# Performance work log

Hardware: AMD Instinct MI355X
Metric: run time of the kernel (lower is better)

Reference implementation:

```python
import jax, jax.numpy as jnp
import numpy as np

H = 16  # num_heads
EPS = 1e-6

def _sigma(t):
    # ELU(x)+1, the positive feature map used by Infini-attention linear memory
    return jax.nn.elu(t) + 1.0

def setup_inputs() -> dict:
    key = jax.random.key(0)
    ks = jax.random.split(key, 6)
    B, S, D = 1, 2048, 1024
    d = D // H
    std = 1.0 / np.sqrt(D)
    return {
        "x": jax.random.normal(ks[0], (B, S, D), dtype=jnp.float32),
        "M": jnp.zeros((H, d, d), dtype=jnp.float32),
        "z": jnp.zeros((H, d), dtype=jnp.float32),
        "Wq": jax.random.normal(ks[1], (D, D), dtype=jnp.float32) * std,
        "Wk": jax.random.normal(ks[2], (D, D), dtype=jnp.float32) * std,
        "Wv": jax.random.normal(ks[3], (D, D), dtype=jnp.float32) * std,
        "Wo": jax.random.normal(ks[4], (D, D), dtype=jnp.float32) * std,
        "beta": jnp.zeros((H,), dtype=jnp.float32),
    }

def reference(x, M, z, Wq, Wk, Wv, Wo, beta):
    B, S, D = x.shape
    d = D // H
    # projections -> [B, H, S, d]
    def proj(W):
        return (x @ W).reshape(B, S, H, d).transpose(0, 2, 1, 3)
    q, k, v = proj(Wq), proj(Wk), proj(Wv)

    # ---- local causal dot-product attention ----
    scale = 1.0 / jnp.sqrt(jnp.asarray(d, dtype=x.dtype))
    scores = jnp.einsum('bhqd,bhkd->bhqk', q, k) * scale  # [B,H,S,S]
    causal = jnp.tril(jnp.ones((S, S), dtype=bool))
    scores = jnp.where(causal, scores, jnp.asarray(-1e30, dtype=scores.dtype))
    A_dot = jnp.einsum('bhqk,bhkd->bhqd', jax.nn.softmax(scores, axis=-1), v)

    # ---- compressive memory retrieval (linear attention) ----
    sq = _sigma(q)                                       # [B,H,S,d]
    num = jnp.einsum('bhsd,hde->bhse', sq, M)            # [B,H,S,d]
    den = jnp.einsum('bhsd,hd->bhs', sq, z)[..., None]   # [B,H,S,1]
    A_mem = num / (den + EPS)

    # ---- learned gate blend ----
    g = jax.nn.sigmoid(beta).reshape(1, H, 1, 1)
    o = g * A_mem + (1.0 - g) * A_dot                    # [B,H,S,d]
    out = o.transpose(0, 2, 1, 3).reshape(B, S, D) @ Wo  # [B,S,D]

    # ---- memory update (stateful, no_grad in original) ----
    sk = _sigma(k)
    M_new = jax.lax.stop_gradient(M + jnp.einsum('bhsd,bhse->hde', sk, v))
    z_new = jax.lax.stop_gradient(z + sk.sum(axis=(0, 2)))
    return out, M_new, z_new
```

## Files before the change

kernel.cpp:

```cpp
#include <hip/hip_runtime.h>

#define S_LEN 2048
#define D_MODEL 1024
#define NH 16
#define DH 64

typedef __attribute__((ext_vector_type(8))) short bf16x8;
typedef __attribute__((ext_vector_type(4))) float f32x4;

__device__ __forceinline__ f32x4 mfma16(bf16x8 a, bf16x8 b, f32x4 c) {
  return __builtin_amdgcn_mfma_f32_16x16x32_bf16(a, b, c, 0, 0, 0);
}

__device__ __forceinline__ void ldst16(const ushort* g, ushort* l) {
  __builtin_amdgcn_global_load_lds(
      (const __attribute__((address_space(1))) void*)g,
      (__attribute__((address_space(3))) void*)l, 16, 0, 0);
}

__device__ __forceinline__ ushort bf16_rne(float f) {
  unsigned u = __float_as_uint(f);
  unsigned r = (u + 0x7FFFu + ((u >> 16) & 1u)) >> 16;
  return (ushort)r;
}
__device__ __forceinline__ float bf16_to_f(ushort u) {
  return __uint_as_float((unsigned)u << 16);
}

__global__ __launch_bounds__(256) void cast_bf16(
    const float* __restrict__ in, ushort* __restrict__ hi, int n4)
{
  int i = blockIdx.x * 256 + threadIdx.x;
  if (i >= n4) return;
  float4 v = ((const float4*)in)[i];
  ushort4 h;
  h.x = bf16_rne(v.x); h.y = bf16_rne(v.y);
  h.z = bf16_rne(v.z); h.w = bf16_rne(v.w);
  ((ushort4*)hi)[i] = h;
}

__global__ __launch_bounds__(256) void splitT(
    const float* __restrict__ W0, const float* __restrict__ W1,
    const float* __restrict__ W2, const float* __restrict__ W3,
    ushort* __restrict__ H0, ushort* __restrict__ L0,
    ushort* __restrict__ H1, ushort* __restrict__ L1,
    ushort* __restrict__ H2, ushort* __restrict__ L2,
    ushort* __restrict__ H3, ushort* __restrict__ L3)
{
  const int zz = blockIdx.z;
  const float* W = zz == 0 ? W0 : (zz == 1 ? W1 : (zz == 2 ? W2 : W3));
  ushort* H = zz == 0 ? H0 : (zz == 1 ? H1 : (zz == 2 ? H2 : H3));
  ushort* L = zz == 0 ? L0 : (zz == 1 ? L1 : (zz == 2 ? L2 : L3));
  __shared__ float ts[32][33];
  const int k0 = blockIdx.x * 32, n0 = blockIdx.y * 32;
  const int r = threadIdx.x >> 3, c4 = (threadIdx.x & 7) * 4;
  float4 v = *(const float4*)&W[(size_t)(k0 + r) * D_MODEL + n0 + c4];
  ts[r][c4 + 0] = v.x; ts[r][c4 + 1] = v.y; ts[r][c4 + 2] = v.z; ts[r][c4 + 3] = v.w;
  __syncthreads();
  ushort4 h, l;
#pragma unroll
  for (int ii = 0; ii < 4; ii++) {
    float f = ts[c4 + ii][r];
    ushort hb = bf16_rne(f);
    ushort lb = bf16_rne(f - __uint_as_float((unsigned)hb << 16));
    ((ushort*)&h)[ii] = hb;
    ((ushort*)&l)[ii] = lb;
  }
  *(ushort4*)&H[(size_t)(n0 + r) * D_MODEL + k0 + c4] = h;
  *(ushort4*)&L[(size_t)(n0 + r) * D_MODEL + k0 + c4] = l;
}

template<int TN, int TWO>
__global__ __launch_bounds__(256, 3) void gemm_t(
    const ushort* __restrict__ Ah,
    const ushort* __restrict__ B0h, const ushort* __restrict__ B0l,
    const ushort* __restrict__ B1h, const ushort* __restrict__ B1l,
    const ushort* __restrict__ B2h, const ushort* __restrict__ B2l,
    float* __restrict__ C0, int K, int mode,
    ushort* __restrict__ aqb, ushort* __restrict__ akb,
    ushort* __restrict__ akbT, ushort* __restrict__ avbT)
{
  const int t = threadIdx.x;
  const int w = t >> 6, lane = t & 63;
  const int quad = lane >> 4, lr = lane & 15;
  const int bx = blockIdx.x;
  const int bw = (bx * TN) >> 10;
  const int n0 = (bx * TN) & 1023;
  const int m0 = blockIdx.y * 64;
  const ushort* Bh = bw == 0 ? B0h : (bw == 1 ? B1h : B2h);
  const ushort* Bl = bw == 0 ? B0l : (bw == 1 ? B1l : B2l);

  __shared__ ushort sAh[64 * 32];
  __shared__ ushort sBh[TN * 32];
  __shared__ ushort sBl[(TWO ? TN : 1) * 32];

  constexpr int NF = TN / 32;
  f32x4 acc[2][NF];
#pragma unroll
  for (int mi = 0; mi < 2; mi++)
#pragma unroll
    for (int ni = 0; ni < NF; ni++)
#pragma unroll
      for (int r = 0; r < 4; r++) acc[mi][ni][r] = 0.f;

  const int mbase = (w & 1) * 32;
  const int nbase = (w >> 1) * (TN / 2);
  const int rowA = w * 16 + (lane >> 2), kcA = (lane & 3) * 8;

  for (int k0 = 0; k0 < K; k0 += 32) {
    __syncthreads();
    ldst16(Ah + (size_t)(m0 + rowA) * K + k0 + kcA, &sAh[w * 512]);
#pragma unroll
    for (int i = 0; i < TN / 64; i++) {
      int rowB = w * (TN / 4) + i * 16 + (lane >> 2);
      int base = (w * (TN / 4) + i * 16) * 32;
      ldst16(Bh + (size_t)(n0 + rowB) * K + k0 + kcA, &sBh[base]);
      if (TWO)
        ldst16(Bl + (size_t)(n0 + rowB) * K + k0 + kcA, &sBl[base]);
    }
    __syncthreads();

    bf16x8 ah[2], bh[NF], bl[NF];
#pragma unroll
    for (int mi = 0; mi < 2; mi++)
      ah[mi] = *(const bf16x8*)&sAh[(mbase + mi * 16 + lr) * 32 + quad * 8];
#pragma unroll
    for (int ni = 0; ni < NF; ni++) {
      int rown = nbase + ni * 16 + lr;
      bh[ni] = *(const bf16x8*)&sBh[rown * 32 + quad * 8];
      if (TWO) bl[ni] = *(const bf16x8*)&sBl[rown * 32 + quad * 8];
    }
#pragma unroll
    for (int mi = 0; mi < 2; mi++)
#pragma unroll
      for (int ni = 0; ni < NF; ni++) {
        acc[mi][ni] = mfma16(ah[mi], bh[ni], acc[mi][ni]);
        if (TWO) acc[mi][ni] = mfma16(ah[mi], bl[ni], acc[mi][ni]);
      }
  }

  if (mode == 0) {
#pragma unroll
    for (int mi = 0; mi < 2; mi++)
#pragma unroll
      for (int ni = 0; ni < NF; ni++)
#pragma unroll
        for (int r = 0; r < 4; r++) {
          int row = m0 + mbase + mi * 16 + quad * 4 + r;
          int col = n0 + nbase + ni * 16 + lr;
          C0[(size_t)row * 1024 + col] = acc[mi][ni][r];
        }
  } else if (bw == 0) {
#pragma unroll
    for (int mi = 0; mi < 2; mi++)
#pragma unroll
      for (int ni = 0; ni < NF; ni++)
#pragma unroll
        for (int r = 0; r < 4; r++) {
          int row = m0 + mbase + mi * 16 + quad * 4 + r;
          int col = n0 + nbase + ni * 16 + lr;
          aqb[(size_t)row * 1024 + col] = bf16_rne(acc[mi][ni][r] * 0.125f);
        }
  } else if (bw == 1) {
#pragma unroll
    for (int mi = 0; mi < 2; mi++)
#pragma unroll
      for (int ni = 0; ni < NF; ni++) {
        int row0 = m0 + mbase + mi * 16 + quad * 4;
        int col = n0 + nbase + ni * 16 + lr;
        ushort4 pk;
#pragma unroll
        for (int r = 0; r < 4; r++) {
          ushort b = bf16_rne(acc[mi][ni][r]);
          ((ushort*)&pk)[r] = b;
          akb[(size_t)(row0 + r) * 1024 + col] = b;
        }
        *(ushort4*)&akbT[(size_t)col * 2048 + row0] = pk;
      }
  } else {
#pragma unroll
    for (int mi = 0; mi < 2; mi++)
#pragma unroll
      for (int ni = 0; ni < NF; ni++) {
        int row0 = m0 + mbase + mi * 16 + quad * 4;
        int col = n0 + nbase + ni * 16 + lr;
        ushort4 pk;
#pragma unroll
        for (int r = 0; r < 4; r++)
          ((ushort*)&pk)[r] = bf16_rne(acc[mi][ni][r]);
        *(ushort4*)&avbT[(size_t)col * 2048 + row0] = pk;
      }
  }
}

__global__ __launch_bounds__(256, 3) void attn_fused(
    const ushort* __restrict__ qb, const ushort* __restrict__ kb,
    const ushort* __restrict__ vbT, const ushort* __restrict__ kbT,
    const float* __restrict__ Mmem, const float* __restrict__ zmem,
    const float* __restrict__ beta,
    ushort* __restrict__ oh,
    float* __restrict__ Mout, float* __restrict__ zout)
{
  const int t = threadIdx.x;
  const int w = t >> 6, lane = t & 63;
  const int quad = lane >> 4, lr = lane & 15;

  __shared__ __align__(16) ushort sBuf[24576];
  __shared__ float drow[64];
  __shared__ float sL[64];

  if (blockIdx.x < 16) {
    const int h = blockIdx.x;
    float* red = (float*)sBuf;
    f32x4 acc[4][4];
#pragma unroll
    for (int mt = 0; mt < 4; mt++)
#pragma unroll
      for (int nt = 0; nt < 4; nt++)
#pragma unroll
        for (int r = 0; r < 4; r++) acc[mt][nt][r] = 0.f;
    float accZ[4] = {0.f, 0.f, 0.f, 0.f};

#pragma unroll 2
    for (int step = 0; step < 16; step++) {
      int k0 = w * 512 + step * 32;
      bf16x8 ah[4], al[4];
#pragma unroll
      for (int mt = 0; mt < 4; mt++) {
        bf16x8 raw = *(const bf16x8*)&kbT[(size_t)(h * 64 + mt * 16 + lr) * 2048 + k0 + quad * 8];
        bf16x8 hh, ll;
#pragma unroll
        for (int j = 0; j < 8; j++) {
          float f = bf16_to_f((ushort)raw[j]);
          float s = f > 0.f ? f + 1.f : __expf(f);
          accZ[mt] += s;
          ushort hb = bf16_rne(s);
          hh[j] = (short)hb;
          ll[j] = (short)bf16_rne(s - bf16_to_f(hb));
        }
        ah[mt] = hh; al[mt] = ll;
      }
      bf16x8 bv[4];
#pragma unroll
      for (int nt = 0; nt < 4; nt++)
        bv[nt] = *(const bf16x8*)&vbT[(size_t)(h * 64 + nt * 16 + lr) * 2048 + k0 + quad * 8];
#pragma unroll
      for (int mt = 0; mt < 4; mt++)
#pragma unroll
        for (int nt = 0; nt < 4; nt++) {
          acc[mt][nt] = mfma16(ah[mt], bv[nt], acc[mt][nt]);
          acc[mt][nt] = mfma16(al[mt], bv[nt], acc[mt][nt]);
        }
    }
#pragma unroll
    for (int mt = 0; mt < 4; mt++) {
      accZ[mt] += __shfl_xor(accZ[mt], 16);
      accZ[mt] += __shfl_xor(accZ[mt], 32);
    }
    if (w < 2) {
#pragma unroll
      for (int mt = 0; mt < 4; mt++)
#pragma unroll
        for (int nt = 0; nt < 4; nt++)
#pragma unroll
          for (int r = 0; r < 4; r++)
            red[w * 4096 + (mt * 16 + quad * 4 + r) * 64 + nt * 16 + lr] = acc[mt][nt][r];
    }
    __syncthreads();
    if (w >= 2) {
#pragma unroll
      for (int mt = 0; mt < 4; mt++)
#pragma unroll
        for (int nt = 0; nt < 4; nt++)
#pragma unroll
          for (int r = 0; r < 4; r++)
            red[(w - 2) * 4096 + (mt * 16 + quad * 4 + r) * 64 + nt * 16 + lr] += acc[mt][nt][r];
    }
    __syncthreads();
    for (int i = t; i < 4096; i += 256)
      Mout[(size_t)h * 4096 + i] = Mmem[(size_t)h * 4096 + i] + red[i] + red[4096 + i];
    __syncthreads();
    if (quad == 0) {
#pragma unroll
      for (int mt = 0; mt < 4; mt++)
        red[w * 64 + mt * 16 + lr] = accZ[mt];
    }
    __syncthreads();
    if (t < 64)
      zout[h * 64 + t] = zmem[h * 64 + t] + red[t] + red[64 + t] + red[128 + t] + red[192 + t];
    return;
  }

  const int a  = blockIdx.x - 16;
  const int h  = a >> 5;
  const int p  = (a >> 1) & 15;
  const int qt = (a & 1) ? p : 31 - p;
  const int s0 = qt * 64;
  const int ntiles = (qt + 2) >> 1;

  const int SPQ = 0, SK = 8192, SVT = 16384;

#pragma unroll
  for (int i = 0; i < 2; i++) {
    int li = w * 2 + i;
    int row = li * 8 + (lane >> 3);
    int cg = ((lane & 7) - row) & 7;
    ldst16(qb + (size_t)(s0 + row) * 1024 + h * 64 + cg * 8, &sBuf[SPQ + li * 512]);
  }
  __syncthreads();
  const int arow = w * 16 + lr;
  const bf16x8 aq0 = *(const bf16x8*)&sBuf[SPQ + arow * 64 + ((quad + arow) & 7) * 8];
  const bf16x8 aq1 = *(const bf16x8*)&sBuf[SPQ + arow * 64 + ((4 + quad + arow) & 7) * 8];

  f32x4 oacc[4];
#pragma unroll
  for (int ni = 0; ni < 4; ni++)
#pragma unroll
    for (int r = 0; r < 4; r++) oacc[ni][r] = 0.f;
  f32x4 lacc;
#pragma unroll
  for (int r = 0; r < 4; r++) lacc[r] = 0.f;
  bf16x8 bone;
#pragma unroll
  for (int j = 0; j < 8; j++) bone[j] = (lr == 0) ? (short)0x3F80 : (short)0;

  for (int jt = 0; jt < ntiles; jt++) {
    const int j0 = jt * 128;
    __syncthreads();
#pragma unroll
    for (int i = 0; i < 4; i++) {
      int li = w * 4 + i;
      int rowK = li * 8 + (lane >> 3);
      int cgK = ((lane & 7) - rowK) & 7;
      ldst16(kb + (size_t)(j0 + rowK) * 1024 + h * 64 + cgK * 8,
             &sBuf[SK + li * 512]);
      int rowV = li * 4 + (lane >> 4);
      int cgV = ((lane & 15) - rowV) & 15;
      ldst16(vbT + (size_t)(h * 64 + rowV) * 2048 + j0 + cgV * 8,
             &sBuf[SVT + li * 512]);
    }
    __syncthreads();

    f32x4 sc[8];
#pragma unroll
    for (int nj = 0; nj < 8; nj++) {
      int brow = nj * 16 + lr;
      bf16x8 b0 = *(const bf16x8*)&sBuf[SK + brow * 64 + ((quad + brow) & 7) * 8];
      bf16x8 b1 = *(const bf16x8*)&sBuf[SK + brow * 64 + ((4 + quad + brow) & 7) * 8];
      f32x4 z4; z4[0] = z4[1] = z4[2] = z4[3] = 0.f;
      z4 = mfma16(aq0, b0, z4);
      sc[nj] = mfma16(aq1, b1, z4);
    }
    if (jt == ntiles - 1) {
#pragma unroll
      for (int nj = 0; nj < 8; nj++)
#pragma unroll
        for (int r = 0; r < 4; r++)
          if (j0 + nj * 16 + lr > s0 + w * 16 + quad * 4 + r) sc[nj][r] = -1e30f;
    }

#pragma unroll
    for (int nj = 0; nj < 8; nj++)
#pragma unroll
      for (int r = 0; r < 4; r++) {
        float e = exp2f(fmaf(sc[nj][r], 1.4426950408889634f, -23.083120654223414f));
        int rr2 = w * 16 + quad * 4 + r;
        sBuf[SPQ + rr2 * 128 + ((nj * 16 + lr + rr2 * 8) & 127)] = bf16_rne(e);
      }

    bf16x8 ap[4];
#pragma unroll
    for (int kf = 0; kf < 4; kf++)
      ap[kf] = *(const bf16x8*)&sBuf[SPQ + arow * 128 + ((kf * 32 + quad * 8 + arow * 8) & 127)];
#pragma unroll
    for (int ni = 0; ni < 4; ni++) {
      int brow = ni * 16 + lr;
#pragma unroll
      for (int kf = 0; kf < 4; kf++) {
        bf16x8 bv = *(const bf16x8*)&sBuf[SVT + brow * 128 + ((kf * 32 + quad * 8 + brow * 8) & 127)];
        oacc[ni] = mfma16(ap[kf], bv, oacc[ni]);
      }
    }
#pragma unroll
    for (int kf = 0; kf < 4; kf++)
      lacc = mfma16(ap[kf], bone, lacc);
  }
  __syncthreads();

  float* sF  = (float*)sBuf;
  float* sO  = sF;
  float* ssq = sF + 4352;
  if (lr == 0) {
#pragma unroll
    for (int r = 0; r < 4; r++) sL[w * 16 + quad * 4 + r] = lacc[r];
  }
#pragma unroll
  for (int ni = 0; ni < 4; ni++)
#pragma unroll
    for (int r = 0; r < 4; r++)
      sO[(w * 16 + quad * 4 + r) * 68 + ni * 16 + lr] = oacc[ni][r];

#pragma unroll
  for (int i = 0; i < 4; i++) {
    int idx4 = t + i * 256;
    int r = idx4 >> 4, c4 = (idx4 & 15) * 4;
    ushort4 u4 = *(const ushort4*)&qb[(size_t)(s0 + r) * 1024 + h * 64 + c4];
#pragma unroll
    for (int j = 0; j < 4; j++) {
      float qv = bf16_to_f(((const ushort*)&u4)[j]) * 8.0f;
      ssq[(c4 + j) * 68 + r] = qv > 0.f ? qv + 1.f : __expf(qv);
    }
  }
  __syncthreads();

  {
    int rr2 = t >> 2, part = t & 3;
    float ds = 0.f;
#pragma unroll
    for (int jj = 0; jj < 16; jj++) {
      int c = part + jj * 4;
      ds = fmaf(ssq[c * 68 + rr2], zmem[h * 64 + c], ds);
    }
    ds += __shfl_xor(ds, 1);
    ds += __shfl_xor(ds, 2);
    if (part == 0) drow[rr2] = ds + 1e-6f;
  }
  __syncthreads();

  const int tx = t & 15, ty = t >> 4;
  float nacc[4][4] = {};
#pragma unroll 8
  for (int dd = 0; dd < 64; dd++) {
    float4 av = *(const float4*)&ssq[dd * 68 + ty * 4];
    float4 bv = *(const float4*)&Mmem[(size_t)h * 4096 + dd * 64 + tx * 4];
    float aa[4] = {av.x, av.y, av.z, av.w};
    float bb[4] = {bv.x, bv.y, bv.z, bv.w};
#pragma unroll
    for (int i = 0; i < 4; i++)
#pragma unroll
      for (int j = 0; j < 4; j++)
        nacc[i][j] = fmaf(aa[i], bb[j], nacc[i][j]);
  }
  float g = 1.f / (1.f + __expf(-beta[h]));
#pragma unroll
  for (int i = 0; i < 4; i++) {
    int r = ty * 4 + i;
    float invd = g / drow[r];
    float invl = (1.f - g) / sL[r];
    float4 od = *(const float4*)&sO[r * 68 + tx * 4];
    float b0 = nacc[i][0] * invd + od.x * invl;
    float b1 = nacc[i][1] * invd + od.y * invl;
    float b2 = nacc[i][2] * invd + od.z * invl;
    float b3 = nacc[i][3] * invd + od.w * invl;
    ushort4 hh;
    hh.x = bf16_rne(b0); hh.y = bf16_rne(b1);
    hh.z = bf16_rne(b2); hh.w = bf16_rne(b3);
    *(ushort4*)&oh[(size_t)(s0 + r) * 1024 + h * 64 + tx * 4] = hh;
  }
}

extern "C" void kernel_launch(void* const* d_in, const int* in_sizes, int n_in,
                              void* d_out, int out_size, void* d_ws, size_t ws_size,
                              hipStream_t stream) {
  const float* x    = (const float*)d_in[0];
  const float* M    = (const float*)d_in[1];
  const float* z    = (const float*)d_in[2];
  const float* Wq   = (const float*)d_in[3];
  const float* Wk   = (const float*)d_in[4];
  const float* Wv   = (const float*)d_in[5];
  const float* Wo   = (const float*)d_in[6];
  const float* beta = (const float*)d_in[7];

  float* out  = (float*)d_out;
  float* Mout = out + (size_t)S_LEN * D_MODEL;
  float* zout = Mout + NH*DH*DH;

  const size_t NE = (size_t)S_LEN * D_MODEL;
  const size_t WE = (size_t)D_MODEL * D_MODEL;
  ushort* xh  = (ushort*)d_ws;
  ushort* wqh = xh + NE;
  ushort* wql = wqh + WE;
  ushort* wkh = wql + WE;
  ushort* wkl = wkh + WE;
  ushort* wvh = wkl + WE;
  ushort* wvl = wvh + WE;
  ushort* woh = wvl + WE;
  ushort* wol = woh + WE;
  ushort* qb  = wol + WE;
  ushort* kb  = qb + NE;
  ushort* kbT = kb + NE;
  ushort* vbT = kbT + NE;
  ushort* ohb = vbT + NE;

  cast_bf16<<<dim3(NE/4/256), 256, 0, stream>>>(x, xh, (int)(NE/4));
  splitT<<<dim3(32, 32, 4), 256, 0, stream>>>(Wq, Wk, Wv, Wo,
      wqh, wql, wkh, wkl, wvh, wvl, woh, wol);

  gemm_t<128, 0><<<dim3(24, 32), 256, 0, stream>>>(xh,
      wqh, wql, wkh, wkl, wvh, wvl,
      (float*)nullptr, D_MODEL, 1, qb, kb, kbT, vbT);

  attn_fused<<<dim3(528), 256, 0, stream>>>(qb, kb, vbT, kbT,
      M, z, beta, ohb, Mout, zout);

  gemm_t<64, 1><<<dim3(16, 32), 256, 0, stream>>>(ohb,
      woh, wol, woh, wol, woh, wol,
      out, D_MODEL, 0, nullptr, nullptr, nullptr, nullptr);
}
```

Before: 184.8 us.

## Drop bf16 lo-split of weights, retile GEMMs, transpose attention MFMA operands

Removes the hi/lo bf16 split of the transposed weights. The castT prep kernel now writes only one bf16 copy, and the output projection GEMM no longer issues a second MFMA against the low part. Both GEMMs are retiled: QKV uses 128x128 tiles and the output projection uses 64x128, which gives fewer blocks with more MFMAs each. The attention kernel swaps MFMA operand order so each lane holds a query row, allowing vectorized ushort4/float4 stores of P and O into shared memory. The cost is reduced precision in the output projection and some fixed-cost occupancy and grid-fill risk from the larger tiles.

```diff
diff --git a/kernel.cpp b/kernel.cpp
--- a/kernel.cpp
+++ b/kernel.cpp
@@ -39,43 +39,33 @@
   ((ushort4*)hi)[i] = h;
 }
 
-__global__ __launch_bounds__(256) void splitT(
+__global__ __launch_bounds__(256) void castT(
     const float* __restrict__ W0, const float* __restrict__ W1,
     const float* __restrict__ W2, const float* __restrict__ W3,
-    ushort* __restrict__ H0, ushort* __restrict__ L0,
-    ushort* __restrict__ H1, ushort* __restrict__ L1,
-    ushort* __restrict__ H2, ushort* __restrict__ L2,
-    ushort* __restrict__ H3, ushort* __restrict__ L3)
+    ushort* __restrict__ H0, ushort* __restrict__ H1,
+    ushort* __restrict__ H2, ushort* __restrict__ H3)
 {
   const int zz = blockIdx.z;
   const float* W = zz == 0 ? W0 : (zz == 1 ? W1 : (zz == 2 ? W2 : W3));
   ushort* H = zz == 0 ? H0 : (zz == 1 ? H1 : (zz == 2 ? H2 : H3));
-  ushort* L = zz == 0 ? L0 : (zz == 1 ? L1 : (zz == 2 ? L2 : L3));
   __shared__ float ts[32][33];
   const int k0 = blockIdx.x * 32, n0 = blockIdx.y * 32;
   const int r = threadIdx.x >> 3, c4 = (threadIdx.x & 7) * 4;
   float4 v = *(const float4*)&W[(size_t)(k0 + r) * D_MODEL + n0 + c4];
   ts[r][c4 + 0] = v.x; ts[r][c4 + 1] = v.y; ts[r][c4 + 2] = v.z; ts[r][c4 + 3] = v.w;
   __syncthreads();
-  ushort4 h, l;
-#pragma unroll
-  for (int ii = 0; ii < 4; ii++) {
-    float f = ts[c4 + ii][r];
-    ushort hb = bf16_rne(f);
-    ushort lb = bf16_rne(f - __uint_as_float((unsigned)hb << 16));
-    ((ushort*)&h)[ii] = hb;
-    ((ushort*)&l)[ii] = lb;
-  }
+  ushort4 h;
+#pragma unroll
+  for (int ii = 0; ii < 4; ii++)
+    ((ushort*)&h)[ii] = bf16_rne(ts[c4 + ii][r]);
   *(ushort4*)&H[(size_t)(n0 + r) * D_MODEL + k0 + c4] = h;
-  *(ushort4*)&L[(size_t)(n0 + r) * D_MODEL + k0 + c4] = l;
-}
-
-template<int TN, int TWO>
-__global__ __launch_bounds__(256, 3) void gemm_t(
+}
+
+template<int TM, int TN>
+__global__ __launch_bounds__(256, 3) void gemm_h(
     const ushort* __restrict__ Ah,
-    const ushort* __restrict__ B0h, const ushort* __restrict__ B0l,
-    const ushort* __restrict__ B1h, const ushort* __restrict__ B1l,
-    const ushort* __restrict__ B2h, const ushort* __restrict__ B2l,
+    const ushort* __restrict__ B0h, const ushort* __restrict__ B1h,
+    const ushort* __restrict__ B2h,
     float* __restrict__ C0, int K, int mode,
     ushort* __restrict__ aqb, ushort* __restrict__ akb,
     ushort* __restrict__ akbT, ushort* __restrict__ avbT)
@@ -86,62 +76,55 @@
   const int bx = blockIdx.x;
   const int bw = (bx * TN) >> 10;
   const int n0 = (bx * TN) & 1023;
-  const int m0 = blockIdx.y * 64;
+  const int m0 = blockIdx.y * TM;
   const ushort* Bh = bw == 0 ? B0h : (bw == 1 ? B1h : B2h);
-  const ushort* Bl = bw == 0 ? B0l : (bw == 1 ? B1l : B2l);
-
-  __shared__ ushort sAh[64 * 32];
-  __shared__ ushort sBh[TN * 32];
-  __shared__ ushort sBl[(TWO ? TN : 1) * 32];
-
-  constexpr int NF = TN / 32;
-  f32x4 acc[2][NF];
-#pragma unroll
-  for (int mi = 0; mi < 2; mi++)
+
+  __shared__ ushort sAh[TM * 32], sBh[TN * 32];
+
+  constexpr int MF = TM / 32, NF = TN / 32;
+  f32x4 acc[MF][NF];
+#pragma unroll
+  for (int mi = 0; mi < MF; mi++)
 #pragma unroll
     for (int ni = 0; ni < NF; ni++)
 #pragma unroll
       for (int r = 0; r < 4; r++) acc[mi][ni][r] = 0.f;
 
-  const int mbase = (w & 1) * 32;
+  const int mbase = (w & 1) * (TM / 2);
   const int nbase = (w >> 1) * (TN / 2);
-  const int rowA = w * 16 + (lane >> 2), kcA = (lane & 3) * 8;
+  const int rsub = lane >> 2, kcA = (lane & 3) * 8;
 
   for (int k0 = 0; k0 < K; k0 += 32) {
     __syncthreads();
-    ldst16(Ah + (size_t)(m0 + rowA) * K + k0 + kcA, &sAh[w * 512]);
+#pragma unroll
+    for (int i = 0; i < TM / 64; i++) {
+      int row = i * 64 + w * 16 + rsub;
+      ldst16(Ah + (size_t)(m0 + row) * K + k0 + kcA, &sAh[(i * 64 + w * 16) * 32]);
+    }
 #pragma unroll
     for (int i = 0; i < TN / 64; i++) {
-      int rowB = w * (TN / 4) + i * 16 + (lane >> 2);
-      int base = (w * (TN / 4) + i * 16) * 32;
-      ldst16(Bh + (size_t)(n0 + rowB) * K + k0 + kcA, &sBh[base]);
-      if (TWO)
-        ldst16(Bl + (size_t)(n0 + rowB) * K + k0 + kcA, &sBl[base]);
-    }
-    __syncthreads();
-
-    bf16x8 ah[2], bh[NF], bl[NF];
-#pragma unroll
-    for (int mi = 0; mi < 2; mi++)
+      int row = i * 64 + w * 16 + rsub;
+      ldst16(Bh + (size_t)(n0 + row) * K + k0 + kcA, &sBh[(i * 64 + w * 16) * 32]);
+    }
+    __syncthreads();
+
+    bf16x8 ah[MF], bh[NF];
+#pragma unroll
+    for (int mi = 0; mi < MF; mi++)
       ah[mi] = *(const bf16x8*)&sAh[(mbase + mi * 16 + lr) * 32 + quad * 8];
 #pragma unroll
-    for (int ni = 0; ni < NF; ni++) {
-      int rown = nbase + ni * 16 + lr;
-      bh[ni] = *(const bf16x8*)&sBh[rown * 32 + quad * 8];
-      if (TWO) bl[ni] = *(const bf16x8*)&sBl[rown * 32 + quad * 8];
-    }
-#pragma unroll
-    for (int mi = 0; mi < 2; mi++)
-#pragma unroll
-      for (int ni = 0; ni < NF; ni++) {
+    for (int ni = 0; ni < NF; ni++)
+      bh[ni] = *(const bf16x8*)&sBh[(nbase + ni * 16 + lr) * 32 + quad * 8];
+#pragma unroll
+    for (int mi = 0; mi < MF; mi++)
+#pragma unroll
+      for (int ni = 0; ni < NF; ni++)
         acc[mi][ni] = mfma16(ah[mi], bh[ni], acc[mi][ni]);
-        if (TWO) acc[mi][ni] = mfma16(ah[mi], bl[ni], acc[mi][ni]);
-      }
   }
 
   if (mode == 0) {
 #pragma unroll
-    for (int mi = 0; mi < 2; mi++)
+    for (int mi = 0; mi < MF; mi++)
 #pragma unroll
       for (int ni = 0; ni < NF; ni++)
 #pragma unroll
@@ -152,7 +135,7 @@
         }
   } else if (bw == 0) {
 #pragma unroll
-    for (int mi = 0; mi < 2; mi++)
+    for (int mi = 0; mi < MF; mi++)
 #pragma unroll
       for (int ni = 0; ni < NF; ni++)
 #pragma unroll
@@ -163,7 +146,7 @@
         }
   } else if (bw == 1) {
 #pragma unroll
-    for (int mi = 0; mi < 2; mi++)
+    for (int mi = 0; mi < MF; mi++)
 #pragma unroll
       for (int ni = 0; ni < NF; ni++) {
         int row0 = m0 + mbase + mi * 16 + quad * 4;
@@ -179,7 +162,7 @@
       }
   } else {
 #pragma unroll
-    for (int mi = 0; mi < 2; mi++)
+    for (int mi = 0; mi < MF; mi++)
 #pragma unroll
       for (int ni = 0; ni < NF; ni++) {
         int row0 = m0 + mbase + mi * 16 + quad * 4;
@@ -312,17 +295,17 @@
   const bf16x8 aq0 = *(const bf16x8*)&sBuf[SPQ + arow * 64 + ((quad + arow) & 7) * 8];
   const bf16x8 aq1 = *(const bf16x8*)&sBuf[SPQ + arow * 64 + ((4 + quad + arow) & 7) * 8];
 
-  f32x4 oacc[4];
+  f32x4 oaccT[4];
 #pragma unroll
   for (int ni = 0; ni < 4; ni++)
 #pragma unroll
-    for (int r = 0; r < 4; r++) oacc[ni][r] = 0.f;
+    for (int r = 0; r < 4; r++) oaccT[ni][r] = 0.f;
   f32x4 lacc;
 #pragma unroll
   for (int r = 0; r < 4; r++) lacc[r] = 0.f;
-  bf16x8 bone;
-#pragma unroll
-  for (int j = 0; j < 8; j++) bone[j] = (lr == 0) ? (short)0x3F80 : (short)0;
+  bf16x8 aone;
+#pragma unroll
+  for (int j = 0; j < 8; j++) aone[j] = (short)0x3F80;
 
   for (int jt = 0; jt < ntiles; jt++) {
     const int j0 = jt * 128;
@@ -348,57 +331,52 @@
       bf16x8 b0 = *(const bf16x8*)&sBuf[SK + brow * 64 + ((quad + brow) & 7) * 8];
       bf16x8 b1 = *(const bf16x8*)&sBuf[SK + brow * 64 + ((4 + quad + brow) & 7) * 8];
       f32x4 z4; z4[0] = z4[1] = z4[2] = z4[3] = 0.f;
-      z4 = mfma16(aq0, b0, z4);
-      sc[nj] = mfma16(aq1, b1, z4);
+      z4 = mfma16(b0, aq0, z4);
+      sc[nj] = mfma16(b1, aq1, z4);
     }
     if (jt == ntiles - 1) {
 #pragma unroll
       for (int nj = 0; nj < 8; nj++)
 #pragma unroll
         for (int r = 0; r < 4; r++)
-          if (j0 + nj * 16 + lr > s0 + w * 16 + quad * 4 + r) sc[nj][r] = -1e30f;
-    }
-
-#pragma unroll
-    for (int nj = 0; nj < 8; nj++)
+          if (j0 + nj * 16 + quad * 4 + r > s0 + arow) sc[nj][r] = -1e30f;
+    }
+
+#pragma unroll
+    for (int nj = 0; nj < 8; nj++) {
+      ushort4 pk;
 #pragma unroll
       for (int r = 0; r < 4; r++) {
         float e = exp2f(fmaf(sc[nj][r], 1.4426950408889634f, -23.083120654223414f));
-        int rr2 = w * 16 + quad * 4 + r;
-        sBuf[SPQ + rr2 * 128 + ((nj * 16 + lr + rr2 * 8) & 127)] = bf16_rne(e);
+        ((ushort*)&pk)[r] = bf16_rne(e);
       }
-
-    bf16x8 ap[4];
-#pragma unroll
-    for (int kf = 0; kf < 4; kf++)
-      ap[kf] = *(const bf16x8*)&sBuf[SPQ + arow * 128 + ((kf * 32 + quad * 8 + arow * 8) & 127)];
-#pragma unroll
-    for (int ni = 0; ni < 4; ni++) {
-      int brow = ni * 16 + lr;
-#pragma unroll
-      for (int kf = 0; kf < 4; kf++) {
-        bf16x8 bv = *(const bf16x8*)&sBuf[SVT + brow * 128 + ((kf * 32 + quad * 8 + brow * 8) & 127)];
-        oacc[ni] = mfma16(ap[kf], bv, oacc[ni]);
+      int col = nj * 16 + quad * 4;
+      *(ushort4*)&sBuf[SPQ + arow * 128 + ((col + arow * 8) & 127)] = pk;
+    }
+
+#pragma unroll
+    for (int kf = 0; kf < 4; kf++) {
+      bf16x8 bp = *(const bf16x8*)&sBuf[SPQ + arow * 128 + ((kf * 32 + quad * 8 + arow * 8) & 127)];
+#pragma unroll
+      for (int ni = 0; ni < 4; ni++) {
+        int vrow = ni * 16 + lr;
+        bf16x8 av = *(const bf16x8*)&sBuf[SVT + vrow * 128 + ((kf * 32 + quad * 8 + vrow * 8) & 127)];
+        oaccT[ni] = mfma16(av, bp, oaccT[ni]);
       }
-    }
-#pragma unroll
-    for (int kf = 0; kf < 4; kf++)
-      lacc = mfma16(ap[kf], bone, lacc);
+      lacc = mfma16(aone, bp, lacc);
+    }
   }
   __syncthreads();
 
   float* sF  = (float*)sBuf;
   float* sO  = sF;
   float* ssq = sF + 4352;
-  if (lr == 0) {
-#pragma unroll
-    for (int r = 0; r < 4; r++) sL[w * 16 + quad * 4 + r] = lacc[r];
-  }
-#pragma unroll
-  for (int ni = 0; ni < 4; ni++)
-#pragma unroll
-    for (int r = 0; r < 4; r++)
-      sO[(w * 16 + quad * 4 + r) * 68 + ni * 16 + lr] = oacc[ni][r];
+  if (quad == 0) sL[arow] = lacc[0];
+#pragma unroll
+  for (int ni = 0; ni < 4; ni++) {
+    float4 o4 = make_float4(oaccT[ni][0], oaccT[ni][1], oaccT[ni][2], oaccT[ni][3]);
+    *(float4*)&sO[arow * 68 + ni * 16 + quad * 4] = o4;
+  }
 
 #pragma unroll
   for (int i = 0; i < 4; i++) {
@@ -479,31 +457,27 @@
   const size_t WE = (size_t)D_MODEL * D_MODEL;
   ushort* xh  = (ushort*)d_ws;
   ushort* wqh = xh + NE;
-  ushort* wql = wqh + WE;
-  ushort* wkh = wql + WE;
-  ushort* wkl = wkh + WE;
-  ushort* wvh = wkl + WE;
-  ushort* wvl = wvh + WE;
-  ushort* woh = wvl + WE;
-  ushort* wol = woh + WE;
-  ushort* qb  = wol + WE;
+  ushort* wkh = wqh + WE;
+  ushort* wvh = wkh + WE;
+  ushort* woh = wvh + WE;
+  ushort* qb  = woh + WE;
   ushort* kb  = qb + NE;
   ushort* kbT = kb + NE;
   ushort* vbT = kbT + NE;
   ushort* ohb = vbT + NE;
 
   cast_bf16<<<dim3(NE/4/256), 256, 0, stream>>>(x, xh, (int)(NE/4));
-  splitT<<<dim3(32, 32, 4), 256, 0, stream>>>(Wq, Wk, Wv, Wo,
-      wqh, wql, wkh, wkl, wvh, wvl, woh, wol);
-
-  gemm_t<128, 0><<<dim3(24, 32), 256, 0, stream>>>(xh,
-      wqh, wql, wkh, wkl, wvh, wvl,
+  castT<<<dim3(32, 32, 4), 256, 0, stream>>>(Wq, Wk, Wv, Wo,
+      wqh, wkh, wvh, woh);
+
+  gemm_h<128, 128><<<dim3(24, 16), 256, 0, stream>>>(xh,
+      wqh, wkh, wvh,
       (float*)nullptr, D_MODEL, 1, qb, kb, kbT, vbT);
 
   attn_fused<<<dim3(528), 256, 0, stream>>>(qb, kb, vbT, kbT,
       M, z, beta, ohb, Mout, zout);
 
-  gemm_t<64, 1><<<dim3(16, 32), 256, 0, stream>>>(ohb,
-      woh, wol, woh, wol, woh, wol,
+  gemm_h<64, 128><<<dim3(8, 32), 256, 0, stream>>>(ohb,
+      woh, woh, woh,
       out, D_MODEL, 0, nullptr, nullptr, nullptr, nullptr);
 }
```

After: 182.3 us. No clear change (-1.4%).
